# Optimization experiments

Hardware: AMD Instinct MI355X
Metric: run time of the kernel (lower is better)

Reference implementation:

```python
import jax, jax.numpy as jnp
import numpy as np
import math

D = 1024
N_HEAD = 16
HEAD_D = D // N_HEAD

def setup_inputs() -> dict:
    key = jax.random.key(0)
    ks = jax.random.split(key, 10)
    b, s = 4, 2048
    scale = 1.0 / math.sqrt(D)
    inp = {
        "decoder_hs": jax.random.normal(ks[0], (b, s, D), dtype=jnp.float32),
        "encoder_hs": jax.random.normal(ks[1], (b, s, D), dtype=jnp.float32),
        "Wq": jax.random.normal(ks[2], (D, D), dtype=jnp.float32) * scale,
        "bq": jnp.zeros((D,), dtype=jnp.float32),
        "Wk": jax.random.normal(ks[3], (D, D), dtype=jnp.float32) * scale,
        "bk": jnp.zeros((D,), dtype=jnp.float32),
        "Wv": jax.random.normal(ks[4], (D, D), dtype=jnp.float32) * scale,
        "bv": jnp.zeros((D,), dtype=jnp.float32),
        "Wp": jax.random.normal(ks[5], (D, D), dtype=jnp.float32) * scale,
        "bp": jnp.zeros((D,), dtype=jnp.float32),
    }
    return inp

def _split_heads(x, b, s):
    # [b, s, d] -> [b, n_head, s, head_d]
    return x.reshape(b, s, N_HEAD, HEAD_D).transpose(0, 2, 1, 3)

def reference(decoder_hs, encoder_hs, Wq, bq, Wk, bk, Wv, bv, Wp, bp):
    b, s, d = decoder_hs.shape
    # torch nn.Linear: y = x @ W.T + b
    q = _split_heads(decoder_hs @ Wq.T + bq, b, s)
    k = _split_heads(encoder_hs @ Wk.T + bk, b, s)
    v = _split_heads(encoder_hs @ Wv.T + bv, b, s)
    att = jnp.einsum('bhqd,bhkd->bhqk', q, k) * (1.0 / math.sqrt(HEAD_D))
    att = jax.nn.softmax(att, axis=-1)  # mask is None, dropout = 0 (eval)
    y = jnp.einsum('bhqk,bhkd->bhqd', att, v)
    y = y.transpose(0, 2, 1, 3).reshape(b, s, d)
    return y @ Wp.T + bp
```

## Files before the change

kernel.cpp:

```cpp
#include <hip/hip_runtime.h>
#include <hip/hip_bf16.h>

typedef __attribute__((ext_vector_type(8))) short bf16x8;
typedef __attribute__((ext_vector_type(4))) float floatx4;
typedef __attribute__((ext_vector_type(16))) float floatx16;
typedef __attribute__((ext_vector_type(2))) int int2v;

#define MFMA_16x16x32(A, B, C) __builtin_amdgcn_mfma_f32_16x16x32_bf16(A, B, C, 0, 0, 0)
#define MFMA_32x32x16(A, B, C) __builtin_amdgcn_mfma_f32_32x32x16_bf16(A, B, C, 0, 0, 0)

__device__ __forceinline__ unsigned short f2b(float f) {
    __hip_bfloat16 h = __float2bfloat16(f);
    unsigned short u;
    __builtin_memcpy(&u, &h, 2);
    return u;
}
__device__ __forceinline__ unsigned pk2(float a, float b) {
    __hip_bfloat162 h = __float22bfloat162_rn(float2{a, b});
    unsigned u;
    __builtin_memcpy(&u, &h, 4);
    return u;
}
__device__ __forceinline__ bf16x8 mk8(int a, int b, int c, int d) {
    union { int u[4]; bf16x8 v; } x;
    x.u[0] = a; x.u[1] = b; x.u[2] = c; x.u[3] = d;
    return x.v;
}
__device__ __forceinline__ void async_lds16(const void* g, void* l) {
    __builtin_amdgcn_global_load_lds((__attribute__((address_space(1))) void*)g,
                                     (__attribute__((address_space(3))) void*)l, 16, 0, 0);
}

struct CvtArgs {
    const float* src[6];
    unsigned short* dst[6];
    float scale[6];
    int n8[6];
};
__global__ __launch_bounds__(256) void convert_kernel(CvtArgs a) {
    const int t = blockIdx.y;
    const int i = blockIdx.x * 256 + threadIdx.x;
    if (i >= a.n8[t]) return;
    const float sc = a.scale[t];
    const float4* s = (const float4*)a.src[t];
    const float4 x = s[2 * i], y = s[2 * i + 1];
    bf16x8 v;
    v[0] = (short)f2b(x.x * sc); v[1] = (short)f2b(x.y * sc);
    v[2] = (short)f2b(x.z * sc); v[3] = (short)f2b(x.w * sc);
    v[4] = (short)f2b(y.x * sc); v[5] = (short)f2b(y.y * sc);
    v[6] = (short)f2b(y.z * sc); v[7] = (short)f2b(y.w * sc);
    *(bf16x8*)(a.dst[t] + (size_t)i * 8) = v;
}

struct QKVArgs {
    const unsigned short* A[3];
    const unsigned short* B[3];
    const float* bias[3];
    float bscale[3];
    unsigned short* C[3];
};
__global__ __launch_bounds__(256, 4) void gemm_qkv(QKVArgs args) {
    constexpr int M = 8192, N = 1024, K = 1024;
    __shared__ __align__(16) unsigned short As[2][4096];
    __shared__ __align__(16) unsigned short Bs[2][4096];

    const int z = blockIdx.z;
    const unsigned short* __restrict__ A = args.A[z];
    const unsigned short* __restrict__ B = args.B[z];
    const float* __restrict__ bias = args.bias[z];
    const float bsc = args.bscale[z];
    unsigned short* __restrict__ C = args.C[z];

    const int tid  = threadIdx.x;
    const int wave = tid >> 6;
    const int lane = tid & 63;
    const int l16  = lane & 15;
    const int quad = lane >> 4;
    const int bm = (blockIdx.x & 63) * 128;
    const int bn = (blockIdx.x >> 6) * 128;
    const int wm = (wave >> 1) * 64;
    const int wn = (wave & 1) * 64;

    const int srow = tid >> 2;
    const int skb  = (((tid & 3) ^ ((tid >> 2) & 3) ^ ((tid >> 4) & 3)) * 8);
    const int cq   = ((quad ^ (l16 & 3) ^ ((l16 >> 2) & 3)) * 8);

    floatx4 acc[4][4] = {};

    auto stage = [&](int buf, int k0) {
        async_lds16(A + (size_t)(bm + srow) * K + skb + k0,      &As[buf][tid * 8]);
        async_lds16(A + (size_t)(bm + 64 + srow) * K + skb + k0, &As[buf][2048 + tid * 8]);
        async_lds16(B + (size_t)(bn + srow) * K + skb + k0,      &Bs[buf][tid * 8]);
        async_lds16(B + (size_t)(bn + 64 + srow) * K + skb + k0, &Bs[buf][2048 + tid * 8]);
    };

    stage(0, 0);
    for (int it = 0; it < K / 32; ++it) {
        __syncthreads();
        if (it + 1 < K / 32) stage((it + 1) & 1, (it + 1) * 32);
        const unsigned short* Ac = &As[it & 1][0];
        const unsigned short* Bc = &Bs[it & 1][0];

        bf16x8 af[4], bfr[4];
        #pragma unroll
        for (int i = 0; i < 4; ++i)
            af[i] = *(const bf16x8*)&Ac[(wm + i * 16 + l16) * 32 + cq];
        #pragma unroll
        for (int j = 0; j < 4; ++j)
            bfr[j] = *(const bf16x8*)&Bc[(wn + j * 16 + l16) * 32 + cq];
        #pragma unroll
        for (int i = 0; i < 4; ++i)
            #pragma unroll
            for (int j = 0; j < 4; ++j)
                acc[i][j] = MFMA_16x16x32(af[i], bfr[j], acc[i][j]);
    }

    if (z == 2) {
        #pragma unroll
        for (int j = 0; j < 4; ++j) {
            const int col = bn + wn + j * 16 + l16;
            const float bv = bias[col] * bsc;
            #pragma unroll
            for (int i = 0; i < 4; ++i) {
                uint2 w;
                w.x = pk2(acc[i][j][0] + bv, acc[i][j][1] + bv);
                w.y = pk2(acc[i][j][2] + bv, acc[i][j][3] + bv);
                const size_t off = (size_t)col * (size_t)M + (bm + wm + i * 16 + quad * 4);
                *(uint2*)&C[off] = w;
            }
        }
    } else {
        #pragma unroll
        for (int i = 0; i < 4; ++i) {
            const int row = bm + wm + i * 16 + quad * 4;
            #pragma unroll
            for (int j = 0; j < 4; ++j) {
                const int col = bn + wn + j * 16 + l16;
                const float bv = bias[col] * bsc;
                #pragma unroll
                for (int r = 0; r < 4; ++r)
                    C[(size_t)(row + r) * N + col] = f2b(acc[i][j][r] + bv);
            }
        }
    }
}

__global__ __launch_bounds__(256, 4) void gemm_out(
    const unsigned short* __restrict__ A, const unsigned short* __restrict__ B,
    const float* __restrict__ bias, float* __restrict__ C,
    int M, int N, int K)
{
    __shared__ __align__(16) unsigned short As[2][4096];
    __shared__ __align__(16) unsigned short Bs[2][4096];

    const int tid  = threadIdx.x;
    const int wave = tid >> 6;
    const int lane = tid & 63;
    const int l16  = lane & 15;
    const int quad = lane >> 4;
    const int bm = (blockIdx.x & 63) * 128;
    const int bn = (blockIdx.x >> 6) * 128;
    const int wm = (wave >> 1) * 64;
    const int wn = (wave & 1) * 64;

    const int srow = tid >> 2;
    const int skb  = (((tid & 3) ^ ((tid >> 2) & 3) ^ ((tid >> 4) & 3)) * 8);
    const int cq   = ((quad ^ (l16 & 3) ^ ((l16 >> 2) & 3)) * 8);

    floatx4 acc[4][4] = {};

    auto stage = [&](int buf, int k0) {
        async_lds16(A + (size_t)(bm + srow) * K + skb + k0,      &As[buf][tid * 8]);
        async_lds16(A + (size_t)(bm + 64 + srow) * K + skb + k0, &As[buf][2048 + tid * 8]);
        async_lds16(B + (size_t)(bn + srow) * K + skb + k0,      &Bs[buf][tid * 8]);
        async_lds16(B + (size_t)(bn + 64 + srow) * K + skb + k0, &Bs[buf][2048 + tid * 8]);
    };

    stage(0, 0);
    for (int it = 0; it < K / 32; ++it) {
        __syncthreads();
        if (it + 1 < K / 32) stage((it + 1) & 1, (it + 1) * 32);
        const unsigned short* Ac = &As[it & 1][0];
        const unsigned short* Bc = &Bs[it & 1][0];

        bf16x8 af[4], bfr[4];
        #pragma unroll
        for (int i = 0; i < 4; ++i)
            af[i] = *(const bf16x8*)&Ac[(wm + i * 16 + l16) * 32 + cq];
        #pragma unroll
        for (int j = 0; j < 4; ++j)
            bfr[j] = *(const bf16x8*)&Bc[(wn + j * 16 + l16) * 32 + cq];
        #pragma unroll
        for (int i = 0; i < 4; ++i)
            #pragma unroll
            for (int j = 0; j < 4; ++j)
                acc[i][j] = MFMA_16x16x32(af[i], bfr[j], acc[i][j]);
    }

    float* Tw = ((wave < 2) ? (float*)&As[0][0] : (float*)&Bs[0][0]) + (wave & 1) * 1024;
    const int rrow = lane >> 2;
    const int rch  = lane & 3;
    #pragma unroll
    for (int i = 0; i < 4; ++i) {
        #pragma unroll
        for (int j = 0; j < 4; ++j) {
            const int col = j * 16 + l16;
            const float bv = bias[bn + wn + col];
            floatx4 v;
            #pragma unroll
            for (int r = 0; r < 4; ++r) v[r] = acc[i][j][r] + bv;
            *(floatx4*)&Tw[col * 16 + ((quad ^ (col & 3)) << 2)] = v;
        }
        const int grow = bm + wm + i * 16 + rrow;
        #pragma unroll
        for (int k = 0; k < 4; ++k) {
            const int c0 = (rch + 4 * k) * 4;
            floatx4 v;
            #pragma unroll
            for (int c = 0; c < 4; ++c) {
                const int col = c0 + c;
                v[c] = Tw[col * 16 + ((((rrow >> 2) ^ col) & 3) << 2) + (rrow & 3)];
            }
            *(floatx4*)&C[(size_t)grow * N + bn + wn + c0] = v;
        }
    }
}

__global__ __launch_bounds__(256, 2) void attn_kernel(
    const unsigned short* __restrict__ Q, const unsigned short* __restrict__ Kg,
    const unsigned short* __restrict__ Vt, unsigned short* __restrict__ Y)
{
    __shared__ __align__(16) unsigned short Ks[2][4096];
    __shared__ __align__(16) unsigned short Vs[2][4096];

    const int tid  = threadIdx.x;
    const int wave = tid >> 6;
    const int lane = tid & 63;
    const int l31  = lane & 31;
    const int hi   = lane >> 5;
    const int x7   = lane & 7;
    const int h4   = ((lane >> 4) & 1) << 2;
    const int bh = blockIdx.x & 63;
    const int qt = blockIdx.x >> 6;
    const int b  = bh >> 4;
    const int h  = bh & 15;
    const int q0 = qt * 256 + wave * 64;
    const size_t base  = ((size_t)b * 2048) * 1024 + (size_t)h * 64;
    const size_t vbase = ((size_t)h * 64) * 8192 + (size_t)b * 2048;

    bf16x8 qf[2][4];
    #pragma unroll
    for (int qb = 0; qb < 2; ++qb) {
        const size_t qrow = base + (size_t)(q0 + qb * 32 + l31) * 1024 + hi * 8;
        #pragma unroll
        for (int ks = 0; ks < 4; ++ks)
            qf[qb][ks] = *(const bf16x8*)&Q[qrow + ks * 16];
    }

    bf16x8 ones;
    #pragma unroll
    for (int e = 0; e < 8; ++e) ones[e] = (short)0x3F80;
    const floatx16 Z16 = {0.f,0.f,0.f,0.f,0.f,0.f,0.f,0.f,
                          0.f,0.f,0.f,0.f,0.f,0.f,0.f,0.f};

    floatx16 o[2][2] = {{Z16, Z16}, {Z16, Z16}};
    floatx16 rs[2]   = {Z16, Z16};

    const int r0  = tid >> 3;
    const int csw = (tid & 7) ^ (r0 & 7) ^ (((tid >> 7) & 1) << 2);

    int co[4];
    #pragma unroll
    for (int ks = 0; ks < 4; ++ks) co[ks] = (((ks * 2 + hi) ^ x7 ^ h4) * 8);
    const int krow = l31 * 64;

    auto stage = [&](int buf, int kv0) {
        async_lds16(&Kg[base + (size_t)(kv0 + r0) * 1024 + csw * 8],      &Ks[buf][tid * 8]);
        async_lds16(&Kg[base + (size_t)(kv0 + 32 + r0) * 1024 + csw * 8], &Ks[buf][2048 + tid * 8]);
        async_lds16(&Vt[vbase + (size_t)r0 * 8192 + kv0 + csw * 8],        &Vs[buf][tid * 8]);
        async_lds16(&Vt[vbase + (size_t)(r0 + 32) * 8192 + kv0 + csw * 8], &Vs[buf][2048 + tid * 8]);
    };

    auto procP = [&](const floatx16& st, bf16x8& paA, bf16x8& paB) {
        float e[16];
        #pragma unroll
        for (int i = 0; i < 16; ++i) e[i] = __builtin_amdgcn_exp2f(st[i]);
        const int w0 = (int)pk2(e[0],  e[1]);
        const int w1 = (int)pk2(e[2],  e[3]);
        const int w2 = (int)pk2(e[4],  e[5]);
        const int w3 = (int)pk2(e[6],  e[7]);
        const int w4 = (int)pk2(e[8],  e[9]);
        const int w5 = (int)pk2(e[10], e[11]);
        const int w6 = (int)pk2(e[12], e[13]);
        const int w7 = (int)pk2(e[14], e[15]);
        const int2v a0 = __builtin_amdgcn_permlane32_swap(w0, w2, false, false);
        const int2v a1 = __builtin_amdgcn_permlane32_swap(w1, w3, false, false);
        const int2v a2 = __builtin_amdgcn_permlane32_swap(w4, w6, false, false);
        const int2v a3 = __builtin_amdgcn_permlane32_swap(w5, w7, false, false);
        paA = mk8(a0.x, a1.x, a0.y, a1.y);
        paB = mk8(a2.x, a3.x, a2.y, a3.y);
    };

    stage(0, 0);
    for (int t = 0; t < 32; ++t) {
        __syncthreads();
        if (t < 31) stage((t + 1) & 1, (t + 1) * 64);
        const unsigned short* Kc = &Ks[t & 1][0];
        const unsigned short* Vc = &Vs[t & 1][0];

        floatx16 st[2][2] = {{Z16, Z16}, {Z16, Z16}};
        __builtin_amdgcn_s_setprio(1);
        #pragma unroll
        for (int ks = 0; ks < 4; ++ks) {
            const bf16x8 kf0 = *(const bf16x8*)&Kc[krow + co[ks]];
            const bf16x8 kf1 = *(const bf16x8*)&Kc[2048 + krow + co[ks]];
            st[0][0] = MFMA_32x32x16(kf0, qf[0][ks], st[0][0]);
            st[0][1] = MFMA_32x32x16(kf0, qf[1][ks], st[0][1]);
            st[1][0] = MFMA_32x32x16(kf1, qf[0][ks], st[1][0]);
            st[1][1] = MFMA_32x32x16(kf1, qf[1][ks], st[1][1]);
        }
        __builtin_amdgcn_s_setprio(0);

        bf16x8 pa[4][2];
        procP(st[0][0], pa[0][0], pa[1][0]);
        procP(st[0][1], pa[0][1], pa[1][1]);
        procP(st[1][0], pa[2][0], pa[3][0]);
        procP(st[1][1], pa[2][1], pa[3][1]);

        __builtin_amdgcn_s_setprio(1);
        #pragma unroll
        for (int f = 0; f < 4; ++f) {
            const bf16x8 v0 = *(const bf16x8*)&Vc[krow + co[f]];
            const bf16x8 v1 = *(const bf16x8*)&Vc[2048 + krow + co[f]];
            #pragma unroll
            for (int qb = 0; qb < 2; ++qb) {
                o[qb][0] = MFMA_32x32x16(pa[f][qb], v0, o[qb][0]);
                o[qb][1] = MFMA_32x32x16(pa[f][qb], v1, o[qb][1]);
                rs[qb]   = MFMA_32x32x16(pa[f][qb], ones, rs[qb]);
            }
        }
        __builtin_amdgcn_s_setprio(0);
    }

    #pragma unroll
    for (int qb = 0; qb < 2; ++qb) {
        #pragma unroll
        for (int g = 0; g < 4; ++g) {
            #pragma unroll
            for (int e2 = 0; e2 < 4; ++e2) {
                const int reg = g * 4 + e2;
                const float inv = 1.0f / rs[qb][reg];
                const size_t row = q0 + qb * 32 + 8 * g + 4 * hi + e2;
                Y[base + row * 1024 + l31]      = f2b(o[qb][0][reg] * inv);
                Y[base + row * 1024 + 32 + l31] = f2b(o[qb][1][reg] * inv);
            }
        }
    }
}

extern "C" void kernel_launch(void* const* d_in, const int* in_sizes, int n_in,
                              void* d_out, int out_size, void* d_ws, size_t ws_size,
                              hipStream_t stream)
{
    const float* dec = (const float*)d_in[0];
    const float* enc = (const float*)d_in[1];
    const float* Wq  = (const float*)d_in[2];
    const float* bq  = (const float*)d_in[3];
    const float* Wk  = (const float*)d_in[4];
    const float* bk  = (const float*)d_in[5];
    const float* Wv  = (const float*)d_in[6];
    const float* bv  = (const float*)d_in[7];
    const float* Wp  = (const float*)d_in[8];
    const float* bp  = (const float*)d_in[9];

    const size_t NTOK = 8192, DM = 1024;
    unsigned short* ws = (unsigned short*)d_ws;
    unsigned short* decB = ws;
    unsigned short* encB = decB + NTOK * DM;
    unsigned short* WqB  = encB + NTOK * DM;
    unsigned short* WkB  = WqB + DM * DM;
    unsigned short* WvB  = WkB + DM * DM;
    unsigned short* WpB  = WvB + DM * DM;
    unsigned short* Qb   = WpB + DM * DM;
    unsigned short* Kb   = Qb + NTOK * DM;
    unsigned short* VtG  = Kb + NTOK * DM;
    unsigned short* Yb   = VtG + NTOK * DM;

    const float C_SM = 0.18033688f;

    CvtArgs a;
    a.src[0] = dec; a.src[1] = enc; a.src[2] = Wq; a.src[3] = Wk; a.src[4] = Wv; a.src[5] = Wp;
    a.dst[0] = decB; a.dst[1] = encB; a.dst[2] = WqB; a.dst[3] = WkB; a.dst[4] = WvB; a.dst[5] = WpB;
    a.scale[0] = 1.f; a.scale[1] = 1.f; a.scale[2] = C_SM;
    a.scale[3] = 1.f; a.scale[4] = 1.f; a.scale[5] = 1.f;
    a.n8[0] = a.n8[1] = (int)(NTOK * DM / 8);
    a.n8[2] = a.n8[3] = a.n8[4] = a.n8[5] = (int)(DM * DM / 8);
    convert_kernel<<<dim3(4096, 6), 256, 0, stream>>>(a);

    QKVArgs qa;
    qa.A[0] = decB; qa.A[1] = encB; qa.A[2] = encB;
    qa.B[0] = WqB;  qa.B[1] = WkB;  qa.B[2] = WvB;
    qa.bias[0] = bq; qa.bias[1] = bk; qa.bias[2] = bv;
    qa.bscale[0] = C_SM; qa.bscale[1] = 1.f; qa.bscale[2] = 1.f;
    qa.C[0] = Qb;   qa.C[1] = Kb;   qa.C[2] = VtG;
    gemm_qkv<<<dim3(512, 1, 3), 256, 0, stream>>>(qa);

    attn_kernel<<<dim3(512), 256, 0, stream>>>(Qb, Kb, VtG, Yb);
    gemm_out<<<dim3(512), 256, 0, stream>>>(Yb, WpB, bp, (float*)d_out, 8192, 1024, 1024);
}
```

Baseline: 309.7 us.

## Enlarge QKV and output GEMM tiles to 256x256 with split-phase pipelined staging

```diff
diff --git a/kernel.cpp b/kernel.cpp
--- a/kernel.cpp
+++ b/kernel.cpp
@@ -59,10 +59,10 @@
     float bscale[3];
     unsigned short* C[3];
 };
-__global__ __launch_bounds__(256, 4) void gemm_qkv(QKVArgs args) {
-    constexpr int M = 8192, N = 1024, K = 1024;
-    __shared__ __align__(16) unsigned short As[2][4096];
-    __shared__ __align__(16) unsigned short Bs[2][4096];
+__global__ __launch_bounds__(512, 2) void gemm_qkv(QKVArgs args) {
+    constexpr int M = 8192, K = 1024;
+    __shared__ __align__(16) unsigned short As[2][16384];
+    __shared__ __align__(16) unsigned short Bs[2][16384];
 
     const int z = blockIdx.z;
     const unsigned short* __restrict__ A = args.A[z];
@@ -76,152 +76,219 @@
     const int lane = tid & 63;
     const int l16  = lane & 15;
     const int quad = lane >> 4;
-    const int bm = (blockIdx.x & 63) * 128;
-    const int bn = (blockIdx.x >> 6) * 128;
-    const int wm = (wave >> 1) * 64;
-    const int wn = (wave & 1) * 64;
-
-    const int srow = tid >> 2;
-    const int skb  = (((tid & 3) ^ ((tid >> 2) & 3) ^ ((tid >> 4) & 3)) * 8);
-    const int cq   = ((quad ^ (l16 & 3) ^ ((l16 >> 2) & 3)) * 8);
-
-    floatx4 acc[4][4] = {};
-
-    auto stage = [&](int buf, int k0) {
-        async_lds16(A + (size_t)(bm + srow) * K + skb + k0,      &As[buf][tid * 8]);
-        async_lds16(A + (size_t)(bm + 64 + srow) * K + skb + k0, &As[buf][2048 + tid * 8]);
-        async_lds16(B + (size_t)(bn + srow) * K + skb + k0,      &Bs[buf][tid * 8]);
-        async_lds16(B + (size_t)(bn + 64 + srow) * K + skb + k0, &Bs[buf][2048 + tid * 8]);
+    const int bm = (blockIdx.x & 31) * 256;
+    const int bn = (blockIdx.x >> 5) * 256;
+    const int wm = (wave >> 2) * 128;
+    const int wn = (wave & 3) * 64;
+
+    const int srow  = tid >> 3;
+    const int sslot = tid & 7;
+
+    floatx4 acc[8][4] = {};
+
+    auto stage_half = [&](int h) {
+        const int tile = h >> 2;
+        const int part = h & 3;
+        const int k0   = tile * 64;
+        const unsigned short* src = (part < 2) ? A : B;
+        unsigned short* dst = (part < 2) ? &As[tile & 1][0] : &Bs[tile & 1][0];
+        const int prow  = (part & 1) * 128;
+        const int gbase = (part < 2) ? bm : bn;
+        #pragma unroll
+        for (int j = 0; j < 2; ++j) {
+            const int r  = prow + j * 64 + srow;
+            const int sc = sslot ^ ((r & 4) | ((r & 8) >> 2));
+            async_lds16(src + (size_t)(gbase + r) * K + k0 + sc * 8,
+                        dst + prow * 64 + j * 4096 + tid * 8);
+        }
     };
 
-    stage(0, 0);
-    for (int it = 0; it < K / 32; ++it) {
-        __syncthreads();
-        if (it + 1 < K / 32) stage((it + 1) & 1, (it + 1) * 32);
-        const unsigned short* Ac = &As[it & 1][0];
-        const unsigned short* Bc = &Bs[it & 1][0];
-
-        bf16x8 af[4], bfr[4];
-        #pragma unroll
-        for (int i = 0; i < 4; ++i)
-            af[i] = *(const bf16x8*)&Ac[(wm + i * 16 + l16) * 32 + cq];
-        #pragma unroll
-        for (int j = 0; j < 4; ++j)
-            bfr[j] = *(const bf16x8*)&Bc[(wn + j * 16 + l16) * 32 + cq];
-        #pragma unroll
-        for (int i = 0; i < 4; ++i)
-            #pragma unroll
-            for (int j = 0; j < 4; ++j)
-                acc[i][j] = MFMA_16x16x32(af[i], bfr[j], acc[i][j]);
+    #pragma unroll
+    for (int h = 0; h < 4; ++h) stage_half(h);
+    asm volatile("s_waitcnt vmcnt(0)" ::: "memory");
+    __builtin_amdgcn_s_barrier();
+    __builtin_amdgcn_sched_barrier(0);
+
+    for (int t = 0; t < 16; ++t) {
+        const unsigned short* Ab = &As[t & 1][0];
+        const unsigned short* Bb = &Bs[t & 1][0];
+        #pragma unroll
+        for (int p = 0; p < 4; ++p) {
+            const int mh = p >> 1, nh = p & 1;
+            bf16x8 af[4][2], bfr[2][2];
+            #pragma unroll
+            for (int i = 0; i < 4; ++i) {
+                const int r  = wm + mh * 64 + i * 16 + l16;
+                const int fr = (r & 4) | ((r & 8) >> 2);
+                #pragma unroll
+                for (int ks = 0; ks < 2; ++ks)
+                    af[i][ks] = *(const bf16x8*)&Ab[r * 64 + ((ks * 4 + quad) ^ fr) * 8];
+            }
+            #pragma unroll
+            for (int n = 0; n < 2; ++n) {
+                const int r  = wn + nh * 32 + n * 16 + l16;
+                const int fr = (r & 4) | ((r & 8) >> 2);
+                #pragma unroll
+                for (int ks = 0; ks < 2; ++ks)
+                    bfr[n][ks] = *(const bf16x8*)&Bb[r * 64 + ((ks * 4 + quad) ^ fr) * 8];
+            }
+            if (t < 15 && p < 2) {
+                stage_half(4 * (t + 1) + 2 * p);
+                stage_half(4 * (t + 1) + 2 * p + 1);
+            }
+            __builtin_amdgcn_s_barrier();
+            asm volatile("s_waitcnt lgkmcnt(0)" ::: "memory");
+            __builtin_amdgcn_sched_barrier(0);
+            __builtin_amdgcn_s_setprio(1);
+            #pragma unroll
+            for (int ks = 0; ks < 2; ++ks)
+                #pragma unroll
+                for (int i = 0; i < 4; ++i)
+                    #pragma unroll
+                    for (int n = 0; n < 2; ++n)
+                        acc[mh * 4 + i][nh * 2 + n] =
+                            MFMA_16x16x32(af[i][ks], bfr[n][ks], acc[mh * 4 + i][nh * 2 + n]);
+            __builtin_amdgcn_s_setprio(0);
+            if (p == 3 && t < 15) asm volatile("s_waitcnt vmcnt(0)" ::: "memory");
+            __builtin_amdgcn_s_barrier();
+            __builtin_amdgcn_sched_barrier(0);
+        }
     }
 
     if (z == 2) {
         #pragma unroll
-        for (int j = 0; j < 4; ++j) {
-            const int col = bn + wn + j * 16 + l16;
+        for (int nj = 0; nj < 4; ++nj) {
+            const int col = bn + wn + (nj >> 1) * 32 + (nj & 1) * 16 + l16;
             const float bv = bias[col] * bsc;
             #pragma unroll
-            for (int i = 0; i < 4; ++i) {
+            for (int mi = 0; mi < 8; ++mi) {
                 uint2 w;
-                w.x = pk2(acc[i][j][0] + bv, acc[i][j][1] + bv);
-                w.y = pk2(acc[i][j][2] + bv, acc[i][j][3] + bv);
-                const size_t off = (size_t)col * (size_t)M + (bm + wm + i * 16 + quad * 4);
+                w.x = pk2(acc[mi][nj][0] + bv, acc[mi][nj][1] + bv);
+                w.y = pk2(acc[mi][nj][2] + bv, acc[mi][nj][3] + bv);
+                const size_t off = (size_t)col * (size_t)M
+                                 + (bm + wm + (mi >> 2) * 64 + (mi & 3) * 16 + quad * 4);
                 *(uint2*)&C[off] = w;
             }
         }
     } else {
-        #pragma unroll
-        for (int i = 0; i < 4; ++i) {
-            const int row = bm + wm + i * 16 + quad * 4;
-            #pragma unroll
-            for (int j = 0; j < 4; ++j) {
-                const int col = bn + wn + j * 16 + l16;
+        constexpr int N = 1024;
+        #pragma unroll
+        for (int mi = 0; mi < 8; ++mi) {
+            const int row = bm + wm + (mi >> 2) * 64 + (mi & 3) * 16 + quad * 4;
+            #pragma unroll
+            for (int nj = 0; nj < 4; ++nj) {
+                const int col = bn + wn + (nj >> 1) * 32 + (nj & 1) * 16 + l16;
                 const float bv = bias[col] * bsc;
                 #pragma unroll
                 for (int r = 0; r < 4; ++r)
-                    C[(size_t)(row + r) * N + col] = f2b(acc[i][j][r] + bv);
-            }
-        }
-    }
-}
-
-__global__ __launch_bounds__(256, 4) void gemm_out(
+                    C[(size_t)(row + r) * N + col] = f2b(acc[mi][nj][r] + bv);
+            }
+        }
+    }
+}
+
+__global__ __launch_bounds__(512, 2) void gemm_out(
     const unsigned short* __restrict__ A, const unsigned short* __restrict__ B,
     const float* __restrict__ bias, float* __restrict__ C,
     int M, int N, int K)
 {
-    __shared__ __align__(16) unsigned short As[2][4096];
-    __shared__ __align__(16) unsigned short Bs[2][4096];
+    __shared__ __align__(16) unsigned short As[2][16384];
+    __shared__ __align__(16) unsigned short Bs[2][16384];
 
     const int tid  = threadIdx.x;
     const int wave = tid >> 6;
     const int lane = tid & 63;
     const int l16  = lane & 15;
     const int quad = lane >> 4;
-    const int bm = (blockIdx.x & 63) * 128;
-    const int bn = (blockIdx.x >> 6) * 128;
-    const int wm = (wave >> 1) * 64;
-    const int wn = (wave & 1) * 64;
-
-    const int srow = tid >> 2;
-    const int skb  = (((tid & 3) ^ ((tid >> 2) & 3) ^ ((tid >> 4) & 3)) * 8);
-    const int cq   = ((quad ^ (l16 & 3) ^ ((l16 >> 2) & 3)) * 8);
-
-    floatx4 acc[4][4] = {};
-
-    auto stage = [&](int buf, int k0) {
-        async_lds16(A + (size_t)(bm + srow) * K + skb + k0,      &As[buf][tid * 8]);
-        async_lds16(A + (size_t)(bm + 64 + srow) * K + skb + k0, &As[buf][2048 + tid * 8]);
-        async_lds16(B + (size_t)(bn + srow) * K + skb + k0,      &Bs[buf][tid * 8]);
-        async_lds16(B + (size_t)(bn + 64 + srow) * K + skb + k0, &Bs[buf][2048 + tid * 8]);
+    const int bm = (blockIdx.x & 31) * 256;
+    const int bn = (blockIdx.x >> 5) * 256;
+    const int wm = (wave >> 2) * 128;
+    const int wn = (wave & 3) * 64;
+
+    const int srow  = tid >> 3;
+    const int sslot = tid & 7;
+
+    floatx4 acc[8][4] = {};
+
+    auto stage_half = [&](int h) {
+        const int tile = h >> 2;
+        const int part = h & 3;
+        const int k0   = tile * 64;
+        const unsigned short* src = (part < 2) ? A : B;
+        unsigned short* dst = (part < 2) ? &As[tile & 1][0] : &Bs[tile & 1][0];
+        const int prow  = (part & 1) * 128;
+        const int gbase = (part < 2) ? bm : bn;
+        #pragma unroll
+        for (int j = 0; j < 2; ++j) {
+            const int r  = prow + j * 64 + srow;
+            const int sc = sslot ^ ((r & 4) | ((r & 8) >> 2));
+            async_lds16(src + (size_t)(gbase + r) * K + k0 + sc * 8,
+                        dst + prow * 64 + j * 4096 + tid * 8);
+        }
     };
 
-    stage(0, 0);
-    for (int it = 0; it < K / 32; ++it) {
-        __syncthreads();
-        if (it + 1 < K / 32) stage((it + 1) & 1, (it + 1) * 32);
-        const unsigned short* Ac = &As[it & 1][0];
-        const unsigned short* Bc = &Bs[it & 1][0];
-
-        bf16x8 af[4], bfr[4];
-        #pragma unroll
-        for (int i = 0; i < 4; ++i)
-            af[i] = *(const bf16x8*)&Ac[(wm + i * 16 + l16) * 32 + cq];
-        #pragma unroll
-        for (int j = 0; j < 4; ++j)
-            bfr[j] = *(const bf16x8*)&Bc[(wn + j * 16 + l16) * 32 + cq];
-        #pragma unroll
-        for (int i = 0; i < 4; ++i)
-            #pragma unroll
-            for (int j = 0; j < 4; ++j)
-                acc[i][j] = MFMA_16x16x32(af[i], bfr[j], acc[i][j]);
-    }
-
-    float* Tw = ((wave < 2) ? (float*)&As[0][0] : (float*)&Bs[0][0]) + (wave & 1) * 1024;
-    const int rrow = lane >> 2;
-    const int rch  = lane & 3;
-    #pragma unroll
-    for (int i = 0; i < 4; ++i) {
-        #pragma unroll
-        for (int j = 0; j < 4; ++j) {
-            const int col = j * 16 + l16;
-            const float bv = bias[bn + wn + col];
-            floatx4 v;
-            #pragma unroll
-            for (int r = 0; r < 4; ++r) v[r] = acc[i][j][r] + bv;
-            *(floatx4*)&Tw[col * 16 + ((quad ^ (col & 3)) << 2)] = v;
-        }
-        const int grow = bm + wm + i * 16 + rrow;
-        #pragma unroll
-        for (int k = 0; k < 4; ++k) {
-            const int c0 = (rch + 4 * k) * 4;
-            floatx4 v;
-            #pragma unroll
-            for (int c = 0; c < 4; ++c) {
-                const int col = c0 + c;
-                v[c] = Tw[col * 16 + ((((rrow >> 2) ^ col) & 3) << 2) + (rrow & 3)];
-            }
-            *(floatx4*)&C[(size_t)grow * N + bn + wn + c0] = v;
+    #pragma unroll
+    for (int h = 0; h < 4; ++h) stage_half(h);
+    asm volatile("s_waitcnt vmcnt(0)" ::: "memory");
+    __builtin_amdgcn_s_barrier();
+    __builtin_amdgcn_sched_barrier(0);
+
+    for (int t = 0; t < 16; ++t) {
+        const unsigned short* Ab = &As[t & 1][0];
+        const unsigned short* Bb = &Bs[t & 1][0];
+        #pragma unroll
+        for (int p = 0; p < 4; ++p) {
+            const int mh = p >> 1, nh = p & 1;
+            bf16x8 af[4][2], bfr[2][2];
+            #pragma unroll
+            for (int i = 0; i < 4; ++i) {
+                const int r  = wm + mh * 64 + i * 16 + l16;
+                const int fr = (r & 4) | ((r & 8) >> 2);
+                #pragma unroll
+                for (int ks = 0; ks < 2; ++ks)
+                    af[i][ks] = *(const bf16x8*)&Ab[r * 64 + ((ks * 4 + quad) ^ fr) * 8];
+            }
+            #pragma unroll
+            for (int n = 0; n < 2; ++n) {
+                const int r  = wn + nh * 32 + n * 16 + l16;
+                const int fr = (r & 4) | ((r & 8) >> 2);
+                #pragma unroll
+                for (int ks = 0; ks < 2; ++ks)
+                    bfr[n][ks] = *(const bf16x8*)&Bb[r * 64 + ((ks * 4 + quad) ^ fr) * 8];
+            }
+            if (t < 15 && p < 2) {
+                stage_half(4 * (t + 1) + 2 * p);
+                stage_half(4 * (t + 1) + 2 * p + 1);
+            }
+            __builtin_amdgcn_s_barrier();
+            asm volatile("s_waitcnt lgkmcnt(0)" ::: "memory");
+            __builtin_amdgcn_sched_barrier(0);
+            __builtin_amdgcn_s_setprio(1);
+            #pragma unroll
+            for (int ks = 0; ks < 2; ++ks)
+                #pragma unroll
+                for (int i = 0; i < 4; ++i)
+                    #pragma unroll
+                    for (int n = 0; n < 2; ++n)
+                        acc[mh * 4 + i][nh * 2 + n] =
+                            MFMA_16x16x32(af[i][ks], bfr[n][ks], acc[mh * 4 + i][nh * 2 + n]);
+            __builtin_amdgcn_s_setprio(0);
+            if (p == 3 && t < 15) asm volatile("s_waitcnt vmcnt(0)" ::: "memory");
+            __builtin_amdgcn_s_barrier();
+            __builtin_amdgcn_sched_barrier(0);
+        }
+    }
+
+    #pragma unroll
+    for (int mi = 0; mi < 8; ++mi) {
+        const int row = bm + wm + (mi >> 2) * 64 + (mi & 3) * 16 + quad * 4;
+        #pragma unroll
+        for (int nj = 0; nj < 4; ++nj) {
+            const int col = bn + wn + (nj >> 1) * 32 + (nj & 1) * 16 + l16;
+            const float bv = bias[col];
+            #pragma unroll
+            for (int r = 0; r < 4; ++r)
+                C[(size_t)(row + r) * N + col] = acc[mi][nj][r] + bv;
         }
     }
 }
@@ -403,8 +470,8 @@
     qa.bias[0] = bq; qa.bias[1] = bk; qa.bias[2] = bv;
     qa.bscale[0] = C_SM; qa.bscale[1] = 1.f; qa.bscale[2] = 1.f;
     qa.C[0] = Qb;   qa.C[1] = Kb;   qa.C[2] = VtG;
-    gemm_qkv<<<dim3(512, 1, 3), 256, 0, stream>>>(qa);
+    gemm_qkv<<<dim3(128, 1, 3), 512, 0, stream>>>(qa);
 
     attn_kernel<<<dim3(512), 256, 0, stream>>>(Qb, Kb, VtG, Yb);
-    gemm_out<<<dim3(512), 256, 0, stream>>>(Yb, WpB, bp, (float*)d_out, 8192, 1024, 1024);
-}
+    gemm_out<<<dim3(128), 512, 0, stream>>>(Yb, WpB, bp, (float*)d_out, 8192, 1024, 1024);
+}
```

After: 359.5 us. +16.1%, slower.
